# Kernel tuning notes

Hardware: AMD Instinct MI355X
Metric: run time of the kernel (lower is better)

Reference implementation:

```python
import jax, jax.numpy as jnp
import numpy as np

EPS = 1e-12

def _dist(a, b):
    # euclidean distance between matching vectors along last axis,
    # computed exactly as pdist_torch: ||a||^2 + ||b||^2 - 2 a.b, clamp, sqrt
    sq = jnp.sum(a * a, -1) + jnp.sum(b * b, -1) - 2.0 * jnp.sum(a * b, -1)
    return jnp.sqrt(jnp.clip(sq, EPS))


def setup_inputs() -> dict:
    key = jax.random.key(0)
    k1, k2 = jax.random.split(key)
    N, D = 8192, 2048
    input1 = jax.random.normal(k1, (N, D), dtype=jnp.float32)
    input2 = jax.random.normal(k2, (N, D), dtype=jnp.float32)
    return {"input1": input1, "input2": input2, "num_pos": 4}


def reference(input1, input2, num_pos):
    N, D = input1.shape
    id_num = N // num_pos
    r = input1.reshape(id_num, num_pos, D)   # RGB features per identity
    ir = input2.reshape(id_num, num_pos, D)  # IR features per identity

    cross_center_rgb = jnp.mean(r, axis=1)   # [id_num, D]
    cross_center_ir = jnpp = jnp.mean(ir, axis=1)

    # leave-one-out intra centers (vectorized): (sum - x) / (num_pos - 1)
    loo_rgb = (jnp.sum(r, axis=1, keepdims=True) - r) / (num_pos - 1)  # [id,pos,D]
    # NOTE: faithful to original bug — intra IR center is also built from RGB feats
    loo_ir = loo_rgb

    d_intra_rgb = _dist(r, loo_rgb)                        # [id, pos]
    d_intra_ir = _dist(ir, loo_ir)
    d_cross_rgb = _dist(r, cross_center_ir[:, None, :])
    d_cross_ir = _dist(ir, cross_center_rgb[:, None, :])

    loss = jnp.sum((d_cross_rgb - d_intra_rgb) ** 2
                   + (d_cross_ir - d_intra_ir) ** 2) / N / 2.0
    return loss
```

## Files before the change

kernel.cpp:

```cpp
#include <hip/hip_runtime.h>
#include <hip/hip_bf16.h>


typedef float f32x4 __attribute__((ext_vector_type(4)));

constexpr int D    = 2048;
constexpr int NPOS = 4;
constexpr int TPB  = 256;
constexpr int NACC = 25;

__global__ void zero_out_kernel(float* out) { out[0] = 0.0f; }

__global__ void __launch_bounds__(TPB, 2) msel_feat_kernel(
        const float* __restrict__ in1,
        const float* __restrict__ in2,
        float* __restrict__ out) {
    const long id = blockIdx.x;
    const float* __restrict__ ra = in1 + id * (long)(NPOS * D);
    const float* __restrict__ rb = in2 + id * (long)(NPOS * D);

    unsigned ofs[8];
#pragma unroll
    for (int p = 0; p < NPOS; ++p) {
#pragma unroll
        for (int h = 0; h < 2; ++h)
            ofs[p * 2 + h] = (unsigned)(p * (D * 4) + h * 4096 + threadIdx.x * 16);
    }

    f32x4 a0, a1, a2, a3, a4, a5, a6, a7;
    f32x4 b0, b1, b2, b3, b4, b5, b6, b7;
#define MSEL_LD(dst, off, base) \
    asm volatile("global_load_dwordx4 %0, %1, %2" : "=v"(dst) : "v"(off), "s"(base))
    MSEL_LD(a0, ofs[0], ra); MSEL_LD(a1, ofs[1], ra);
    MSEL_LD(a2, ofs[2], ra); MSEL_LD(a3, ofs[3], ra);
    MSEL_LD(a4, ofs[4], ra); MSEL_LD(a5, ofs[5], ra);
    MSEL_LD(a6, ofs[6], ra); MSEL_LD(a7, ofs[7], ra);
    MSEL_LD(b0, ofs[0], rb); MSEL_LD(b1, ofs[1], rb);
    MSEL_LD(b2, ofs[2], rb); MSEL_LD(b3, ofs[3], rb);
    MSEL_LD(b4, ofs[4], rb); MSEL_LD(b5, ofs[5], rb);
    MSEL_LD(b6, ofs[6], rb); MSEL_LD(b7, ofs[7], rb);
#undef MSEL_LD

    asm volatile("s_waitcnt vmcnt(0)"
                 : "+v"(a0), "+v"(a1), "+v"(a2), "+v"(a3),
                   "+v"(a4), "+v"(a5), "+v"(a6), "+v"(a7),
                   "+v"(b0), "+v"(b1), "+v"(b2), "+v"(b3),
                   "+v"(b4), "+v"(b5), "+v"(b6), "+v"(b7));
    __builtin_amdgcn_sched_barrier(0);

    const f32x4 rA[2][NPOS] = {{a0, a2, a4, a6}, {a1, a3, a5, a7}};
    const f32x4 iA[2][NPOS] = {{b0, b2, b4, b6}, {b1, b3, b5, b7}};

    float acc[NACC];
#pragma unroll
    for (int k = 0; k < NACC; ++k) acc[k] = 0.0f;

#pragma unroll
    for (int h = 0; h < 2; ++h) {
#pragma unroll
        for (int e = 0; e < 4; ++e) {
            const float x0 = rA[h][0][e], x1 = rA[h][1][e],
                        x2 = rA[h][2][e], x3 = rA[h][3][e];
            const float y0 = iA[h][0][e], y1 = iA[h][1][e],
                        y2 = iA[h][2][e], y3 = iA[h][3][e];
            const float s = x0 + x1 + x2 + x3;
            const float t = y0 + y1 + y2 + y3;
            const float x[NPOS] = {x0, x1, x2, x3};
            const float y[NPOS] = {y0, y1, y2, y3};
            acc[24] = fmaf(t, t, acc[24]);
#pragma unroll
            for (int p = 0; p < NPOS; ++p) {
                acc[0  + p] = fmaf(x[p], x[p], acc[0  + p]);
                acc[4  + p] = fmaf(y[p], y[p], acc[4  + p]);
                acc[8  + p] = fmaf(s,    x[p], acc[8  + p]);
                acc[12 + p] = fmaf(s,    y[p], acc[12 + p]);
                acc[16 + p] = fmaf(x[p], y[p], acc[16 + p]);
                acc[20 + p] = fmaf(x[p], t,    acc[20 + p]);
            }
        }
    }

#pragma unroll
    for (int k = 0; k < NACC; ++k) {
        float v = acc[k];
#pragma unroll
        for (int off = 32; off > 0; off >>= 1) v += __shfl_down(v, off, 64);
        acc[k] = v;
    }

    __shared__ float lds[TPB / 64][NACC];
    const int wave = threadIdx.x >> 6;
    const int lane = threadIdx.x & 63;
    if (lane == 0) {
#pragma unroll
        for (int k = 0; k < NACC; ++k) lds[wave][k] = acc[k];
    }
    __syncthreads();

    if (threadIdx.x == 0) {
        float tot[NACC];
#pragma unroll
        for (int k = 0; k < NACC; ++k)
            tot[k] = lds[0][k] + lds[1][k] + lds[2][k] + lds[3][k];

        const float ss = tot[8] + tot[9] + tot[10] + tot[11];
        const float tt = tot[24];
        float contrib = 0.0f;
#pragma unroll
        for (int p = 0; p < NPOS; ++p) {
            const float rr = tot[0 + p];
            const float ii = tot[4 + p];
            const float sr = tot[8 + p];
            const float si = tot[12 + p];
            const float ri = tot[16 + p];
            const float rt = tot[20 + p];

            const float b2loo = (ss - 2.0f * sr + rr) * (1.0f / 9.0f);
            const float sq_intra_rgb = rr + b2loo - 2.0f * ((sr - rr) * (1.0f / 3.0f));
            const float sq_intra_ir  = ii + b2loo - 2.0f * ((si - ri) * (1.0f / 3.0f));
            const float sq_cross_rgb = rr + tt * 0.0625f - 0.5f * rt;
            const float sq_cross_ir  = ii + ss * 0.0625f - 0.5f * si;

            const float d_ir_rgb = sqrtf(fmaxf(sq_intra_rgb, 1e-12f));
            const float d_ir_ir  = sqrtf(fmaxf(sq_intra_ir,  1e-12f));
            const float d_cr_rgb = sqrtf(fmaxf(sq_cross_rgb, 1e-12f));
            const float d_cr_ir  = sqrtf(fmaxf(sq_cross_ir,  1e-12f));

            const float e1 = d_cr_rgb - d_ir_rgb;
            const float e2 = d_cr_ir  - d_ir_ir;
            contrib += e1 * e1 + e2 * e2;
        }
        atomicAdd(out, contrib * (1.0f / 16384.0f));
    }
}

extern "C" void kernel_launch(void* const* d_in, const int* in_sizes, int n_in,
                              void* d_out, int out_size, void* d_ws, size_t ws_size,
                              hipStream_t stream) {
    const float* in1 = (const float*)d_in[0];
    const float* in2 = (const float*)d_in[1];
    float* out = (float*)d_out;

    const int id_num = in_sizes[0] / (NPOS * D);

    zero_out_kernel<<<1, 1, 0, stream>>>(out);
    msel_feat_kernel<<<id_num, TPB, 0, stream>>>(in1, in2, out);
}
```

Baseline: 150.7 us.

## Process four identities per block with double-buffered loads and a separate epilogue

Each block now handles four identities and double-buffers the register loads, so the next identity's global loads are in flight while the current one is reduced. Per-wave partial sums go to a zeroed workspace through atomics instead of an LDS reduction with __syncthreads, and a second kernel computes the distances and the final sum. The goal is to hide memory latency and drop the block barrier. The cost is a workspace memset, an extra kernel launch, 25 global atomics per wave per identity, and higher register pressure from the two buffers.

```diff
diff --git a/kernel.cpp b/kernel.cpp
--- a/kernel.cpp
+++ b/kernel.cpp
@@ -8,104 +8,117 @@
 constexpr int NPOS = 4;
 constexpr int TPB  = 256;
 constexpr int NACC = 25;
+constexpr int IDS  = 4;
 
 __global__ void zero_out_kernel(float* out) { out[0] = 0.0f; }
 
-__global__ void __launch_bounds__(TPB, 2) msel_feat_kernel(
+__global__ void __launch_bounds__(TPB, 2) msel_partial_kernel(
         const float* __restrict__ in1,
         const float* __restrict__ in2,
-        float* __restrict__ out) {
-    const long id = blockIdx.x;
-    const float* __restrict__ ra = in1 + id * (long)(NPOS * D);
-    const float* __restrict__ rb = in2 + id * (long)(NPOS * D);
+        float* __restrict__ ws,
+        int id_num) {
+    const long id0 = (long)blockIdx.x * IDS;
+    const float* a_base = in1 + id0 * (long)(NPOS * D);
+    const float* b_base = in2 + id0 * (long)(NPOS * D);
 
     unsigned ofs[8];
 #pragma unroll
-    for (int p = 0; p < NPOS; ++p) {
+    for (int p = 0; p < NPOS; ++p)
 #pragma unroll
         for (int h = 0; h < 2; ++h)
             ofs[p * 2 + h] = (unsigned)(p * (D * 4) + h * 4096 + threadIdx.x * 16);
-    }
 
-    f32x4 a0, a1, a2, a3, a4, a5, a6, a7;
-    f32x4 b0, b1, b2, b3, b4, b5, b6, b7;
-#define MSEL_LD(dst, off, base) \
-    asm volatile("global_load_dwordx4 %0, %1, %2" : "=v"(dst) : "v"(off), "s"(base))
-    MSEL_LD(a0, ofs[0], ra); MSEL_LD(a1, ofs[1], ra);
-    MSEL_LD(a2, ofs[2], ra); MSEL_LD(a3, ofs[3], ra);
-    MSEL_LD(a4, ofs[4], ra); MSEL_LD(a5, ofs[5], ra);
-    MSEL_LD(a6, ofs[6], ra); MSEL_LD(a7, ofs[7], ra);
-    MSEL_LD(b0, ofs[0], rb); MSEL_LD(b1, ofs[1], rb);
-    MSEL_LD(b2, ofs[2], rb); MSEL_LD(b3, ofs[3], rb);
-    MSEL_LD(b4, ofs[4], rb); MSEL_LD(b5, ofs[5], rb);
-    MSEL_LD(b6, ofs[6], rb); MSEL_LD(b7, ofs[7], rb);
-#undef MSEL_LD
+    f32x4 A0[8], B0[8], A1[8], B1[8];
 
-    asm volatile("s_waitcnt vmcnt(0)"
-                 : "+v"(a0), "+v"(a1), "+v"(a2), "+v"(a3),
-                   "+v"(a4), "+v"(a5), "+v"(a6), "+v"(a7),
-                   "+v"(b0), "+v"(b1), "+v"(b2), "+v"(b3),
-                   "+v"(b4), "+v"(b5), "+v"(b6), "+v"(b7));
-    __builtin_amdgcn_sched_barrier(0);
+    auto issue = [&](f32x4 (&A)[8], f32x4 (&B)[8], int k) {
+        const float* ra = a_base + (long)k * (NPOS * D);
+        const float* rb = b_base + (long)k * (NPOS * D);
+#pragma unroll
+        for (int j = 0; j < 8; ++j)
+            asm volatile("global_load_dwordx4 %0, %1, %2"
+                         : "=v"(A[j]) : "v"(ofs[j]), "s"(ra));
+#pragma unroll
+        for (int j = 0; j < 8; ++j)
+            asm volatile("global_load_dwordx4 %0, %1, %2"
+                         : "=v"(B[j]) : "v"(ofs[j]), "s"(rb));
+    };
 
-    const f32x4 rA[2][NPOS] = {{a0, a2, a4, a6}, {a1, a3, a5, a7}};
-    const f32x4 iA[2][NPOS] = {{b0, b2, b4, b6}, {b1, b3, b5, b7}};
+#define MSEL_WAIT(cnt, A, B)                                                   \
+    asm volatile("s_waitcnt vmcnt(" #cnt ")"                                   \
+                 : "+v"(A[0]), "+v"(A[1]), "+v"(A[2]), "+v"(A[3]),             \
+                   "+v"(A[4]), "+v"(A[5]), "+v"(A[6]), "+v"(A[7]),             \
+                   "+v"(B[0]), "+v"(B[1]), "+v"(B[2]), "+v"(B[3]),             \
+                   "+v"(B[4]), "+v"(B[5]), "+v"(B[6]), "+v"(B[7]));            \
+    __builtin_amdgcn_sched_barrier(0)
 
-    float acc[NACC];
+    auto process = [&](const f32x4 (&A)[8], const f32x4 (&B)[8], long id) {
+        float acc[NACC];
 #pragma unroll
-    for (int k = 0; k < NACC; ++k) acc[k] = 0.0f;
-
+        for (int k = 0; k < NACC; ++k) acc[k] = 0.0f;
 #pragma unroll
-    for (int h = 0; h < 2; ++h) {
+        for (int h = 0; h < 2; ++h) {
 #pragma unroll
-        for (int e = 0; e < 4; ++e) {
-            const float x0 = rA[h][0][e], x1 = rA[h][1][e],
-                        x2 = rA[h][2][e], x3 = rA[h][3][e];
-            const float y0 = iA[h][0][e], y1 = iA[h][1][e],
-                        y2 = iA[h][2][e], y3 = iA[h][3][e];
-            const float s = x0 + x1 + x2 + x3;
-            const float t = y0 + y1 + y2 + y3;
-            const float x[NPOS] = {x0, x1, x2, x3};
-            const float y[NPOS] = {y0, y1, y2, y3};
-            acc[24] = fmaf(t, t, acc[24]);
+            for (int e = 0; e < 4; ++e) {
+                const float x0 = A[0 * 2 + h][e], x1 = A[1 * 2 + h][e],
+                            x2 = A[2 * 2 + h][e], x3 = A[3 * 2 + h][e];
+                const float y0 = B[0 * 2 + h][e], y1 = B[1 * 2 + h][e],
+                            y2 = B[2 * 2 + h][e], y3 = B[3 * 2 + h][e];
+                const float s = x0 + x1 + x2 + x3;
+                const float t = y0 + y1 + y2 + y3;
+                const float x[NPOS] = {x0, x1, x2, x3};
+                const float y[NPOS] = {y0, y1, y2, y3};
+                acc[24] = fmaf(t, t, acc[24]);
 #pragma unroll
-            for (int p = 0; p < NPOS; ++p) {
-                acc[0  + p] = fmaf(x[p], x[p], acc[0  + p]);
-                acc[4  + p] = fmaf(y[p], y[p], acc[4  + p]);
-                acc[8  + p] = fmaf(s,    x[p], acc[8  + p]);
-                acc[12 + p] = fmaf(s,    y[p], acc[12 + p]);
-                acc[16 + p] = fmaf(x[p], y[p], acc[16 + p]);
-                acc[20 + p] = fmaf(x[p], t,    acc[20 + p]);
+                for (int p = 0; p < NPOS; ++p) {
+                    acc[0  + p] = fmaf(x[p], x[p], acc[0  + p]);
+                    acc[4  + p] = fmaf(y[p], y[p], acc[4  + p]);
+                    acc[8  + p] = fmaf(s,    x[p], acc[8  + p]);
+                    acc[12 + p] = fmaf(s,    y[p], acc[12 + p]);
+                    acc[16 + p] = fmaf(x[p], y[p], acc[16 + p]);
+                    acc[20 + p] = fmaf(x[p], t,    acc[20 + p]);
+                }
             }
         }
-    }
+#pragma unroll
+        for (int k = 0; k < NACC; ++k) {
+            float v = acc[k];
+#pragma unroll
+            for (int off = 32; off > 0; off >>= 1) v += __shfl_down(v, off, 64);
+            acc[k] = v;
+        }
+        if ((threadIdx.x & 63) == 0) {
+#pragma unroll
+            for (int k = 0; k < NACC; ++k)
+                atomicAdd(ws + (long)k * id_num + id, acc[k]);
+        }
+    };
 
-#pragma unroll
-    for (int k = 0; k < NACC; ++k) {
-        float v = acc[k];
-#pragma unroll
-        for (int off = 32; off > 0; off >>= 1) v += __shfl_down(v, off, 64);
-        acc[k] = v;
-    }
+    issue(A0, B0, 0);
+    issue(A1, B1, 1);
+    MSEL_WAIT(16, A0, B0);
+    process(A0, B0, id0 + 0);
+    issue(A0, B0, 2);
+    MSEL_WAIT(16, A1, B1);
+    process(A1, B1, id0 + 1);
+    issue(A1, B1, 3);
+    MSEL_WAIT(16, A0, B0);
+    process(A0, B0, id0 + 2);
+    MSEL_WAIT(0, A1, B1);
+    process(A1, B1, id0 + 3);
+#undef MSEL_WAIT
+}
 
-    __shared__ float lds[TPB / 64][NACC];
-    const int wave = threadIdx.x >> 6;
-    const int lane = threadIdx.x & 63;
-    if (lane == 0) {
-#pragma unroll
-        for (int k = 0; k < NACC; ++k) lds[wave][k] = acc[k];
-    }
-    __syncthreads();
-
-    if (threadIdx.x == 0) {
+__global__ void __launch_bounds__(TPB) msel_epilogue_kernel(
+        const float* __restrict__ ws, float* __restrict__ out, int id_num) {
+    const int id = blockIdx.x * TPB + threadIdx.x;
+    float contrib = 0.0f;
+    if (id < id_num) {
         float tot[NACC];
 #pragma unroll
-        for (int k = 0; k < NACC; ++k)
-            tot[k] = lds[0][k] + lds[1][k] + lds[2][k] + lds[3][k];
+        for (int k = 0; k < NACC; ++k) tot[k] = ws[(long)k * id_num + id];
 
         const float ss = tot[8] + tot[9] + tot[10] + tot[11];
         const float tt = tot[24];
-        float contrib = 0.0f;
 #pragma unroll
         for (int p = 0; p < NPOS; ++p) {
             const float rr = tot[0 + p];
@@ -130,8 +143,16 @@
             const float e2 = d_cr_ir  - d_ir_ir;
             contrib += e1 * e1 + e2 * e2;
         }
-        atomicAdd(out, contrib * (1.0f / 16384.0f));
+        contrib *= (1.0f / 16384.0f);
     }
+
+#pragma unroll
+    for (int off = 32; off > 0; off >>= 1) contrib += __shfl_down(contrib, off, 64);
+    __shared__ float lds[TPB / 64];
+    if ((threadIdx.x & 63) == 0) lds[threadIdx.x >> 6] = contrib;
+    __syncthreads();
+    if (threadIdx.x == 0)
+        atomicAdd(out, lds[0] + lds[1] + lds[2] + lds[3]);
 }
 
 extern "C" void kernel_launch(void* const* d_in, const int* in_sizes, int n_in,
@@ -140,9 +161,12 @@
     const float* in1 = (const float*)d_in[0];
     const float* in2 = (const float*)d_in[1];
     float* out = (float*)d_out;
+    float* ws  = (float*)d_ws;
 
     const int id_num = in_sizes[0] / (NPOS * D);
 
+    hipMemsetAsync(ws, 0, (size_t)NACC * id_num * sizeof(float), stream);
     zero_out_kernel<<<1, 1, 0, stream>>>(out);
-    msel_feat_kernel<<<id_num, TPB, 0, stream>>>(in1, in2, out);
+    msel_partial_kernel<<<id_num / IDS, TPB, 0, stream>>>(in1, in2, ws, id_num);
+    msel_epilogue_kernel<<<(id_num + TPB - 1) / TPB, TPB, 0, stream>>>(ws, out, id_num);
 }
```

Measured after the change: 161.5 us. +7.2%, slower.
